# Performance work log

Measured on AMD Instinct MI355X. Metric: run time of the kernel, lower is better.

Reference implementation:

```python
import jax, jax.numpy as jnp
import numpy as np

# Model dims (match init_kwargs): dim=768, num_heads=12, num_kv_heads=2 -> G=6, head_dim=64
DIM, HKV, G, D = 768, 2, 6, 64


def setup_inputs() -> dict:
    key = jax.random.key(0)
    ks = jax.random.split(key, 9)
    w = 0.02  # init scale for weights
    return {
        "x": jax.random.normal(ks[0], (8, 1024, DIM), dtype=jnp.float32),
        "depth_k": jax.random.normal(ks[1], (8, 1024, HKV, D), dtype=jnp.float32),
        "depth_v": jax.random.normal(ks[2], (8, 1024, HKV, D), dtype=jnp.float32),
        "Wq": jax.random.normal(ks[3], (DIM, DIM), dtype=jnp.float32) * w,
        "bq": jnp.zeros((DIM,), dtype=jnp.float32),
        "Wkv": jax.random.normal(ks[4], (2 * HKV * D, DIM), dtype=jnp.float32) * w,
        "bkv": jnp.zeros((2 * HKV * D,), dtype=jnp.float32),
        "Wproj": jax.random.normal(ks[5], (DIM, DIM), dtype=jnp.float32) * w,
        "bproj": jnp.zeros((DIM,), dtype=jnp.float32),
    }


def reference(x, depth_k, depth_v, Wq, bq, Wkv, bkv, Wproj, bproj):
    B, N, C = x.shape
    scale = D ** -0.5
    # Q projection, GQA groups unfolded into the sequence dim: [B, N*G, Hkv, D]
    q = (x @ Wq.T + bq).reshape(B, N * G, HKV, D)
    # KV projection: [B, N, 2, Hkv, D]
    kv = (x @ Wkv.T + bkv).reshape(B, N, 2, HKV, D)
    k, v = kv[:, :, 0], kv[:, :, 1]
    # Concatenate depth (previous-layer) KV cache along the sequence dim
    k_full = jnp.concatenate([depth_k, k], axis=1)  # [B, N_cache+N, Hkv, D]
    v_full = jnp.concatenate([depth_v, v], axis=1)
    # Full (non-causal) attention per kv head over the unfolded query sequence
    scores = jnp.einsum('bqhd,bkhd->bhqk', q, k_full) * scale  # [B, Hkv, N*G, Kv]
    attn = jax.nn.softmax(scores, axis=-1)
    o = jnp.einsum('bhqk,bkhd->bqhd', attn, v_full)  # [B, N*G, Hkv, D]
    out = o.reshape(B, N, C) @ Wproj.T + bproj  # fold G*Hkv*D back to C=dim
    return out, k, v
```

## Files before the change

### kernel.cpp

```cpp
#include <hip/hip_runtime.h>

using sh8 = __attribute__((ext_vector_type(8))) short;
using sh4 = __attribute__((ext_vector_type(4))) short;
using fx4 = __attribute__((ext_vector_type(4))) float;

#define MFMA(a,b,c)   __builtin_amdgcn_mfma_f32_16x16x32_bf16((a),(b),(c),0,0,0)
#define MFMA16(a,b,c) __builtin_amdgcn_mfma_f32_16x16x16bf16_1k((a),(b),(c),0,0,0)

__device__ __forceinline__ short f2bf(float f) {
    union { float f; unsigned u; } v; v.f = f;
    return (short)((v.u + 0x7fffu + ((v.u >> 16) & 1u)) >> 16);
}

__device__ __forceinline__ unsigned bfpair(float lo, float hi) {
    unsigned ul = __float_as_uint(lo) + 0x8000u;
    unsigned uh = __float_as_uint(hi) + 0x8000u;
    return __builtin_amdgcn_perm(uh, ul, 0x07060302);
}

__device__ __forceinline__ sh8 pack8(float4 a, float4 b) {
    union { unsigned u[4]; sh8 s; } r;
    r.u[0] = bfpair(a.x, a.y);
    r.u[1] = bfpair(a.z, a.w);
    r.u[2] = bfpair(b.x, b.y);
    r.u[3] = bfpair(b.z, b.w);
    return r.s;
}

#define QSCALE 0.18033688011112042f


__global__ __launch_bounds__(256) void qgemm_k(const float* __restrict__ x,
                                               const float* __restrict__ Wq,
                                               const float* __restrict__ bq,
                                               short* __restrict__ q_ws)
{
    __shared__ alignas(16) short Al[128 * 40];
    __shared__ alignas(16) short Bl[128 * 40];
    const int t    = threadIdx.x;
    const int wave = t >> 6, lane = t & 63;
    const int wm   = wave >> 1, wn = wave & 1;
    const int lhi  = lane >> 4, llo = lane & 15;
    const int bm   = blockIdx.y * 128, bn = blockIdx.x * 128;

    const int srow = t >> 1, scol = (t & 1) * 16;
    const float* ap = x  + (size_t)(bm + srow) * 768 + scol;
    const float* bp = Wq + (size_t)(bn + srow) * 768 + scol;

    fx4 zero = {0.f, 0.f, 0.f, 0.f};
    fx4 acc[4][4];
    #pragma unroll
    for (int i = 0; i < 4; ++i)
        #pragma unroll
        for (int j = 0; j < 4; ++j) acc[i][j] = zero;

    float4 pa0 = *(const float4*)(ap);     float4 pa1 = *(const float4*)(ap + 4);
    float4 pa2 = *(const float4*)(ap + 8); float4 pa3 = *(const float4*)(ap + 12);
    float4 pb0 = *(const float4*)(bp);     float4 pb1 = *(const float4*)(bp + 4);
    float4 pb2 = *(const float4*)(bp + 8); float4 pb3 = *(const float4*)(bp + 12);

    for (int k0 = 0; k0 < 768; k0 += 32) {
        __syncthreads();
        *(sh8*)&Al[srow*40 + scol]     = pack8(pa0, pa1);
        *(sh8*)&Al[srow*40 + scol + 8] = pack8(pa2, pa3);
        *(sh8*)&Bl[srow*40 + scol]     = pack8(pb0, pb1);
        *(sh8*)&Bl[srow*40 + scol + 8] = pack8(pb2, pb3);
        __syncthreads();
        if (k0 + 32 < 768) {
            pa0 = *(const float4*)(ap + k0+32);     pa1 = *(const float4*)(ap + k0+36);
            pa2 = *(const float4*)(ap + k0+40);     pa3 = *(const float4*)(ap + k0+44);
            pb0 = *(const float4*)(bp + k0+32);     pb1 = *(const float4*)(bp + k0+36);
            pb2 = *(const float4*)(bp + k0+40);     pb3 = *(const float4*)(bp + k0+44);
        }
        sh8 af[4], bf[4];
        #pragma unroll
        for (int mt = 0; mt < 4; ++mt)
            af[mt] = *(const sh8*)&Al[(wm*64 + mt*16 + llo)*40 + lhi*8];
        #pragma unroll
        for (int nt = 0; nt < 4; ++nt)
            bf[nt] = *(const sh8*)&Bl[(wn*64 + nt*16 + llo)*40 + lhi*8];
        #pragma unroll
        for (int mt = 0; mt < 4; ++mt)
            #pragma unroll
            for (int nt = 0; nt < 4; ++nt)
                acc[mt][nt] = MFMA(af[mt], bf[nt], acc[mt][nt]);
    }

    #pragma unroll
    for (int nt = 0; nt < 4; ++nt) {
        const int c = bn + wn*64 + nt*16 + llo;
        const float bias = bq[c];
        const int g = c >> 7, h = (c >> 6) & 1, d = c & 63;
        #pragma unroll
        for (int mt = 0; mt < 4; ++mt) {
            const int m0 = bm + wm*64 + mt*16 + lhi*4;
            #pragma unroll
            for (int r = 0; r < 4; ++r) {
                const int m = m0 + r;
                const int b = m >> 10, n = m & 1023;
                const float val = (acc[mt][nt][r] + bias) * QSCALE;
                q_ws[((size_t)(b*2 + h)*6144 + n*6 + g)*64 + d] = f2bf(val);
            }
        }
    }
}

__global__ __launch_bounds__(256) void kvgemm_k(const float* __restrict__ x,
                                                const float* __restrict__ Wkv,
                                                const float* __restrict__ bkv,
                                                float* __restrict__ ok,
                                                float* __restrict__ ov,
                                                short* __restrict__ k_ws,
                                                short* __restrict__ vT_ws)
{
    __shared__ alignas(16) short Al[128 * 40];
    __shared__ alignas(16) short Bl[128 * 40];
    const int t    = threadIdx.x;
    const int wave = t >> 6, lane = t & 63;
    const int wm   = wave >> 1, wn = wave & 1;
    const int lhi  = lane >> 4, llo = lane & 15;
    const int bm   = blockIdx.y * 128, bn = blockIdx.x * 128;

    const int srow = t >> 1, scol = (t & 1) * 16;
    const float* ap = x   + (size_t)(bm + srow) * 768 + scol;
    const float* bp = Wkv + (size_t)(bn + srow) * 768 + scol;

    fx4 zero = {0.f, 0.f, 0.f, 0.f};
    fx4 acc[4][4];
    #pragma unroll
    for (int i = 0; i < 4; ++i)
        #pragma unroll
        for (int j = 0; j < 4; ++j) acc[i][j] = zero;

    float4 pa0 = *(const float4*)(ap);     float4 pa1 = *(const float4*)(ap + 4);
    float4 pa2 = *(const float4*)(ap + 8); float4 pa3 = *(const float4*)(ap + 12);
    float4 pb0 = *(const float4*)(bp);     float4 pb1 = *(const float4*)(bp + 4);
    float4 pb2 = *(const float4*)(bp + 8); float4 pb3 = *(const float4*)(bp + 12);

    for (int k0 = 0; k0 < 768; k0 += 32) {
        __syncthreads();
        *(sh8*)&Al[srow*40 + scol]     = pack8(pa0, pa1);
        *(sh8*)&Al[srow*40 + scol + 8] = pack8(pa2, pa3);
        *(sh8*)&Bl[srow*40 + scol]     = pack8(pb0, pb1);
        *(sh8*)&Bl[srow*40 + scol + 8] = pack8(pb2, pb3);
        __syncthreads();
        if (k0 + 32 < 768) {
            pa0 = *(const float4*)(ap + k0+32);     pa1 = *(const float4*)(ap + k0+36);
            pa2 = *(const float4*)(ap + k0+40);     pa3 = *(const float4*)(ap + k0+44);
            pb0 = *(const float4*)(bp + k0+32);     pb1 = *(const float4*)(bp + k0+36);
            pb2 = *(const float4*)(bp + k0+40);     pb3 = *(const float4*)(bp + k0+44);
        }
        sh8 af[4], bf[4];
        #pragma unroll
        for (int mt = 0; mt < 4; ++mt)
            af[mt] = *(const sh8*)&Al[(wm*64 + mt*16 + llo)*40 + lhi*8];
        #pragma unroll
        for (int nt = 0; nt < 4; ++nt)
            bf[nt] = *(const sh8*)&Bl[(wn*64 + nt*16 + llo)*40 + lhi*8];
        #pragma unroll
        for (int mt = 0; mt < 4; ++mt)
            #pragma unroll
            for (int nt = 0; nt < 4; ++nt)
                acc[mt][nt] = MFMA(af[mt], bf[nt], acc[mt][nt]);
    }

    #pragma unroll
    for (int nt = 0; nt < 4; ++nt) {
        const int c = bn + wn*64 + nt*16 + llo;
        const float bias = bkv[c];
        const int s = c >> 7, h = (c >> 6) & 1, d = c & 63;
        #pragma unroll
        for (int mt = 0; mt < 4; ++mt) {
            const int m0 = bm + wm*64 + mt*16 + lhi*4;
            const int b = m0 >> 10, n0 = m0 & 1023;
            float vals[4];
            #pragma unroll
            for (int r = 0; r < 4; ++r) vals[r] = acc[mt][nt][r] + bias;
            if (s == 0) {
                #pragma unroll
                for (int r = 0; r < 4; ++r) {
                    ok[((size_t)(b*1024 + n0 + r)*2 + h)*64 + d] = vals[r];
                    k_ws[((size_t)(b*2 + h)*2048 + 1024 + n0 + r)*64 + d] = f2bf(vals[r]);
                }
            } else {
                #pragma unroll
                for (int r = 0; r < 4; ++r)
                    ov[((size_t)(b*1024 + n0 + r)*2 + h)*64 + d] = vals[r];
                short4 pk = make_short4(f2bf(vals[0]), f2bf(vals[1]),
                                        f2bf(vals[2]), f2bf(vals[3]));
                *(short4*)&vT_ws[((size_t)((b*2 + h)*64 + d))*2048 + 1024 + n0] = pk;
            }
        }
    }
}

__global__ __launch_bounds__(256) void castdepth_k(const float* __restrict__ dk,
                                                   const float* __restrict__ dv,
                                                   short* __restrict__ k_ws,
                                                   short* __restrict__ vT_ws)
{
    const int t = threadIdx.x;
    if (blockIdx.x < 1024) {
        const size_t idx4 = ((size_t)blockIdx.x * 256 + t) * 4;
        const int b  = (int)(idx4 >> 17);
        const int rm = (int)(idx4 & 131071);
        const int tt = rm >> 7, h = (rm >> 6) & 1, d = rm & 63;
        float4 v = *(const float4*)(dk + idx4);
        short4 pk = make_short4(f2bf(v.x), f2bf(v.y), f2bf(v.z), f2bf(v.w));
        *(short4*)&k_ws[((size_t)(b*2 + h)*2048 + tt)*64 + d] = pk;
    } else {
        __shared__ alignas(16) short tl[64][72];
        const int tile = blockIdx.x - 1024;
        const int bh = tile >> 4, tb = tile & 15;
        const int b = bh >> 1, h = bh & 1, t0 = tb * 64;
        const int tt = t >> 2, d0 = (t & 3) * 16;
        const float* src = dv + ((size_t)(b*1024 + t0 + tt)*2 + h)*64 + d0;
        float4 v0 = *(const float4*)(src);
        float4 v1 = *(const float4*)(src + 4);
        float4 v2 = *(const float4*)(src + 8);
        float4 v3 = *(const float4*)(src + 12);
        *(sh8*)&tl[tt][d0]     = pack8(v0, v1);
        *(sh8*)&tl[tt][d0 + 8] = pack8(v2, v3);
        __syncthreads();
        const int d = t >> 2, ts0 = (t & 3) * 16;
        sh8 o0, o1;
        #pragma unroll
        for (int i = 0; i < 8; ++i) o0[i] = tl[ts0 + i][d];
        #pragma unroll
        for (int i = 0; i < 8; ++i) o1[i] = tl[ts0 + 8 + i][d];
        short* dst = vT_ws + ((size_t)((b*2 + h)*64 + d))*2048 + t0 + ts0;
        *(sh8*)dst       = o0;
        *(sh8*)(dst + 8) = o1;
    }
}

__global__ __launch_bounds__(256) void attn_k(const short* __restrict__ q_ws,
                                              const short* __restrict__ k_ws,
                                              const short* __restrict__ vT_ws,
                                              short* __restrict__ o_ws)
{
    __shared__ alignas(16) short Kl[64][72];
    __shared__ alignas(16) short Vt[64][72];
    const int t    = threadIdx.x;
    const int wave = t >> 6, lane = t & 63;
    const int lhi  = lane >> 4, llo = lane & 15;
    const int bh   = blockIdx.y;
    const int b    = bh >> 1, h = bh & 1;
    const int qt   = blockIdx.x;

    const short* qb = q_ws + ((size_t)bh*6144 + qt*128 + wave*32) * 64;
    sh8 qf[2][2];
    #pragma unroll
    for (int s = 0; s < 2; ++s) {
        qf[s][0] = *(const sh8*)(qb + (s*16 + llo)*64 + lhi*8);
        qf[s][1] = *(const sh8*)(qb + (s*16 + llo)*64 + lhi*8 + 32);
    }

    const short* kbase = k_ws  + (size_t)bh * 2048 * 64;
    const short* vbase = vT_ws + (size_t)bh * 64 * 2048;

    fx4 zero = {0.f, 0.f, 0.f, 0.f};
    fx4 oacc[2][4];
    #pragma unroll
    for (int s = 0; s < 2; ++s)
        #pragma unroll
        for (int dt = 0; dt < 4; ++dt) oacc[s][dt] = zero;
    float lsum[2] = {0.f, 0.f};

    for (int kb = 0; kb < 32; ++kb) {
        __syncthreads();
        #pragma unroll
        for (int i = 0; i < 2; ++i) {
            const int u = t + 256*i;
            const int row = u >> 3, sg = (u & 7) * 8;
            *(sh8*)&Kl[row][sg] = *(const sh8*)(kbase + (size_t)kb*4096 + u*8);
            *(sh8*)&Vt[row][sg] = *(const sh8*)(vbase + (size_t)row*2048 + kb*64 + sg);
        }
        __syncthreads();

        #pragma unroll
        for (int nt = 0; nt < 4; ++nt) {
            sh8 kf0 = *(const sh8*)&Kl[nt*16 + llo][lhi*8];
            sh8 kf1 = *(const sh8*)&Kl[nt*16 + llo][lhi*8 + 32];
            sh4 vt[4];
            #pragma unroll
            for (int dt = 0; dt < 4; ++dt)
                vt[dt] = *(const sh4*)&Vt[dt*16 + llo][nt*16 + lhi*4];
            #pragma unroll
            for (int s = 0; s < 2; ++s) {
                fx4 st = MFMA(kf0, qf[s][0], zero);
                st     = MFMA(kf1, qf[s][1], st);
                float p0 = __builtin_amdgcn_exp2f(st[0]);
                float p1 = __builtin_amdgcn_exp2f(st[1]);
                float p2 = __builtin_amdgcn_exp2f(st[2]);
                float p3 = __builtin_amdgcn_exp2f(st[3]);
                lsum[s] += (p0 + p1) + (p2 + p3);
                union { unsigned u[2]; sh4 s4; } pu;
                pu.u[0] = bfpair(p0, p1);
                pu.u[1] = bfpair(p2, p3);
                #pragma unroll
                for (int dt = 0; dt < 4; ++dt)
                    oacc[s][dt] = MFMA16(pu.s4, vt[dt], oacc[s][dt]);
            }
        }
    }

    float inv[2];
    #pragma unroll
    for (int s = 0; s < 2; ++s) {
        float v = lsum[s];
        v += __shfl_xor(v, 16, 64);
        v += __shfl_xor(v, 32, 64);
        inv[s] = 1.0f / v;
    }

    #pragma unroll
    for (int s = 0; s < 2; ++s) {
        #pragma unroll
        for (int r = 0; r < 4; ++r) {
            const float iq = __shfl(inv[s], lhi*4 + r, 64);
            const int qi = qt*128 + wave*32 + s*16 + lhi*4 + r;
            const int n = qi / 6, g = qi % 6;
            short* orow = o_ws + ((size_t)(b*1024 + n))*768 + g*128 + h*64;
            #pragma unroll
            for (int dt = 0; dt < 4; ++dt)
                orow[dt*16 + llo] = f2bf(oacc[s][dt][r] * iq);
        }
    }
}

__global__ __launch_bounds__(256) void projgemm_k(const short* __restrict__ o_ws,
                                                  const float* __restrict__ Wp,
                                                  const float* __restrict__ bpj,
                                                  float* __restrict__ out)
{
    __shared__ alignas(16) short Al[128 * 40];
    __shared__ alignas(16) short Bl[128 * 40];
    const int t    = threadIdx.x;
    const int wave = t >> 6, lane = t & 63;
    const int wm   = wave >> 1, wn = wave & 1;
    const int lhi  = lane >> 4, llo = lane & 15;
    const int bm   = blockIdx.y * 128, bn = blockIdx.x * 128;

    const int srow = t >> 1, scol = (t & 1) * 16;
    const short* ap = o_ws + (size_t)(bm + srow) * 768 + scol;
    const float* bp = Wp   + (size_t)(bn + srow) * 768 + scol;

    fx4 zero = {0.f, 0.f, 0.f, 0.f};
    fx4 acc[4][4];
    #pragma unroll
    for (int i = 0; i < 4; ++i)
        #pragma unroll
        for (int j = 0; j < 4; ++j) acc[i][j] = zero;

    sh8 qa0 = *(const sh8*)(ap), qa1 = *(const sh8*)(ap + 8);
    float4 pb0 = *(const float4*)(bp);     float4 pb1 = *(const float4*)(bp + 4);
    float4 pb2 = *(const float4*)(bp + 8); float4 pb3 = *(const float4*)(bp + 12);

    for (int k0 = 0; k0 < 768; k0 += 32) {
        __syncthreads();
        *(sh8*)&Al[srow*40 + scol]     = qa0;
        *(sh8*)&Al[srow*40 + scol + 8] = qa1;
        *(sh8*)&Bl[srow*40 + scol]     = pack8(pb0, pb1);
        *(sh8*)&Bl[srow*40 + scol + 8] = pack8(pb2, pb3);
        __syncthreads();
        if (k0 + 32 < 768) {
            qa0 = *(const sh8*)(ap + k0+32);  qa1 = *(const sh8*)(ap + k0+40);
            pb0 = *(const float4*)(bp + k0+32);  pb1 = *(const float4*)(bp + k0+36);
            pb2 = *(const float4*)(bp + k0+40);  pb3 = *(const float4*)(bp + k0+44);
        }
        sh8 af[4], bf[4];
        #pragma unroll
        for (int mt = 0; mt < 4; ++mt)
            af[mt] = *(const sh8*)&Al[(wm*64 + mt*16 + llo)*40 + lhi*8];
        #pragma unroll
        for (int nt = 0; nt < 4; ++nt)
            bf[nt] = *(const sh8*)&Bl[(wn*64 + nt*16 + llo)*40 + lhi*8];
        #pragma unroll
        for (int mt = 0; mt < 4; ++mt)
            #pragma unroll
            for (int nt = 0; nt < 4; ++nt)
                acc[mt][nt] = MFMA(af[mt], bf[nt], acc[mt][nt]);
    }

    #pragma unroll
    for (int nt = 0; nt < 4; ++nt) {
        const int c = bn + wn*64 + nt*16 + llo;
        const float bias = bpj[c];
        #pragma unroll
        for (int mt = 0; mt < 4; ++mt) {
            const int m0 = bm + wm*64 + mt*16 + lhi*4;
            #pragma unroll
            for (int r = 0; r < 4; ++r)
                out[(size_t)(m0 + r)*768 + c] = acc[mt][nt][r] + bias;
        }
    }
}

extern "C" void kernel_launch(void* const* d_in, const int* in_sizes, int n_in,
                              void* d_out, int out_size, void* d_ws, size_t ws_size,
                              hipStream_t stream)
{
    const float* x   = (const float*)d_in[0];
    const float* dk  = (const float*)d_in[1];
    const float* dv  = (const float*)d_in[2];
    const float* Wq  = (const float*)d_in[3];
    const float* bq  = (const float*)d_in[4];
    const float* Wkv = (const float*)d_in[5];
    const float* bkv = (const float*)d_in[6];
    const float* Wp  = (const float*)d_in[7];
    const float* bpj = (const float*)d_in[8];

    float* out = (float*)d_out;
    float* ok  = out + 6291456;
    float* ov  = out + 7340032;

    char* ws = (char*)d_ws;
    short* q_ws  = (short*)(ws);
    short* k_ws  = (short*)(ws + 12582912);
    short* vT_ws = (short*)(ws + 16777216);
    short* o_ws  = (short*)(ws + 20971520);

    qgemm_k    <<<dim3(6, 64), 256, 0, stream>>>(x, Wq, bq, q_ws);
    kvgemm_k   <<<dim3(2, 64), 256, 0, stream>>>(x, Wkv, bkv, ok, ov, k_ws, vT_ws);
    castdepth_k<<<dim3(1280),  256, 0, stream>>>(dk, dv, k_ws, vT_ws);
    attn_k     <<<dim3(48, 16), 256, 0, stream>>>(q_ws, k_ws, vT_ws, o_ws);
    projgemm_k <<<dim3(6, 64), 256, 0, stream>>>(o_ws, Wp, bpj, out);
}
```

Measured before the change: 250.3 us.

## Register-prefetch next K/V tile and permute V smem layout for wide reads

```diff
diff --git a/kernel.cpp b/kernel.cpp
--- a/kernel.cpp
+++ b/kernel.cpp
@@ -26,6 +26,9 @@
     r.u[3] = bfpair(b.z, b.w);
     return r.s;
 }
+
+__device__ __forceinline__ sh4 lo4(sh8 v) { return __builtin_shufflevector(v, v, 0, 1, 2, 3); }
+__device__ __forceinline__ sh4 hi4(sh8 v) { return __builtin_shufflevector(v, v, 4, 5, 6, 7); }
 
 #define QSCALE 0.18033688011112042f
 
@@ -259,6 +262,17 @@
     const short* kbase = k_ws  + (size_t)bh * 2048 * 64;
     const short* vbase = vT_ws + (size_t)bh * 64 * 2048;
 
+    const int urow = t >> 3, uc = t & 7;
+    const int vc1  = ((uc & 1) * 2) * 16 + (uc >> 1) * 4;
+
+    const short* kp = kbase + t * 8;
+    const short* vp = vbase + (size_t)urow * 2048 + uc * 8;
+
+    sh8 kpre0 = *(const sh8*)(kp);
+    sh8 kpre1 = *(const sh8*)(kp + 2048);
+    sh8 vpre0 = *(const sh8*)(vp);
+    sh8 vpre1 = *(const sh8*)(vp + 65536);
+
     fx4 zero = {0.f, 0.f, 0.f, 0.f};
     fx4 oacc[2][4];
     #pragma unroll
@@ -269,23 +283,34 @@
 
     for (int kb = 0; kb < 32; ++kb) {
         __syncthreads();
-        #pragma unroll
-        for (int i = 0; i < 2; ++i) {
-            const int u = t + 256*i;
-            const int row = u >> 3, sg = (u & 7) * 8;
-            *(sh8*)&Kl[row][sg] = *(const sh8*)(kbase + (size_t)kb*4096 + u*8);
-            *(sh8*)&Vt[row][sg] = *(const sh8*)(vbase + (size_t)row*2048 + kb*64 + sg);
-        }
-        __syncthreads();
+        *(sh8*)&Kl[urow][uc*8]         = kpre0;
+        *(sh8*)&Kl[urow + 32][uc*8]    = kpre1;
+        *(sh4*)&Vt[urow][vc1]          = lo4(vpre0);
+        *(sh4*)&Vt[urow][vc1 + 16]     = hi4(vpre0);
+        *(sh4*)&Vt[urow + 32][vc1]     = lo4(vpre1);
+        *(sh4*)&Vt[urow + 32][vc1 + 16]= hi4(vpre1);
+        __syncthreads();
+
+        if (kb < 31) {
+            kpre0 = *(const sh8*)(kp + (kb+1)*4096);
+            kpre1 = *(const sh8*)(kp + (kb+1)*4096 + 2048);
+            vpre0 = *(const sh8*)(vp + (kb+1)*64);
+            vpre1 = *(const sh8*)(vp + (kb+1)*64 + 65536);
+        }
+
+        sh4 vts[4][4];
+        #pragma unroll
+        for (int dt = 0; dt < 4; ++dt) {
+            sh8 va = *(const sh8*)&Vt[dt*16 + llo][lhi*16];
+            sh8 vb = *(const sh8*)&Vt[dt*16 + llo][lhi*16 + 8];
+            vts[0][dt] = lo4(va); vts[1][dt] = hi4(va);
+            vts[2][dt] = lo4(vb); vts[3][dt] = hi4(vb);
+        }
 
         #pragma unroll
         for (int nt = 0; nt < 4; ++nt) {
             sh8 kf0 = *(const sh8*)&Kl[nt*16 + llo][lhi*8];
             sh8 kf1 = *(const sh8*)&Kl[nt*16 + llo][lhi*8 + 32];
-            sh4 vt[4];
-            #pragma unroll
-            for (int dt = 0; dt < 4; ++dt)
-                vt[dt] = *(const sh4*)&Vt[dt*16 + llo][nt*16 + lhi*4];
             #pragma unroll
             for (int s = 0; s < 2; ++s) {
                 fx4 st = MFMA(kf0, qf[s][0], zero);
@@ -300,7 +325,7 @@
                 pu.u[1] = bfpair(p2, p3);
                 #pragma unroll
                 for (int dt = 0; dt < 4; ++dt)
-                    oacc[s][dt] = MFMA16(pu.s4, vt[dt], oacc[s][dt]);
+                    oacc[s][dt] = MFMA16(pu.s4, vts[nt][dt], oacc[s][dt]);
             }
         }
     }
```

Measured after the change: 254.3 us. No clear change (+1.6%).
